# Performance work log

Measured on AMD Instinct MI355X. Metric: run time of the kernel, lower is better.

## Reference

```python
import jax, jax.numpy as jnp
import numpy as np

SCALE = 1.0  # module scale=1; dropout_p=0 so dropout is identity; selector is Identity


def setup_inputs() -> dict:
    key = jax.random.key(0)
    k0, k1, k2, k3, k4 = jax.random.split(key, 5)
    B, S, DIN, DOUT, P, R = 4, 2048, 4096, 4096, 5, 8
    x = jax.random.normal(k0, (B, S, DIN), dtype=jnp.float32)
    W = jax.random.normal(k1, (DOUT, DIN), dtype=jnp.float32) * 0.02   # nn.Linear weight [out, in]
    lora_down = jax.random.normal(k2, (P, DIN, R), dtype=jnp.float32) * 0.02
    lora_up = jax.random.normal(k3, (P, R, DOUT), dtype=jnp.float32) * 0.02
    lora_route = jax.random.normal(k4, (P, DIN, P), dtype=jnp.float32) * 0.02
    return {"x": x, "W": W, "lora_down": lora_down, "lora_up": lora_up,
            "lora_route": lora_route, "task_id": 4}


def reference(x, W, lora_down, lora_up, lora_route, task_id):
    tid = task_id  # Python int (static), tid > 1 branch
    # Routing: logits over the first (tid-1) experts using route table of task tid
    logits = jnp.einsum('bsi,ij->bsj', x, lora_route[tid - 1, :, :tid - 1])  # [B,S,tid-1]
    omegas = jax.nn.softmax(logits, axis=-1)
    # Previous experts: (lora_down[j] @ lora_up[j]).detach() -> stop_gradient.
    # Keep low-rank structure: z = x @ down  [B,S,J,R], then weight and project up.
    down_prev = jax.lax.stop_gradient(lora_down[:tid - 1])  # [J, DIN, R]
    up_prev = jax.lax.stop_gradient(lora_up[:tid - 1])      # [J, R, DOUT]
    z = jnp.einsum('bsi,jir->bsjr', x, down_prev)           # [B,S,J,R] small (R=8)
    delta_prev = jnp.einsum('bsjr,jro->bso', z * omegas[..., None], up_prev)
    # Current expert (j == tid-1): live params, no gating weight
    cur = (x @ lora_down[tid - 1]) @ lora_up[tid - 1]       # [B,S,DOUT]
    delta = SCALE * (delta_prev + cur)
    return x @ W.T + delta
```

## Files before the change

### kernel.cpp

```cpp
#include <hip/hip_runtime.h>
#include <hip/hip_bf16.h>

typedef unsigned short u16;
typedef __attribute__((ext_vector_type(8))) __bf16 bf16x8;
typedef __attribute__((ext_vector_type(4))) float f32x4;

#define DIN 4096
#define DOUT 4096
#define MROWS 8192

__device__ __forceinline__ u16 f2bf(float f) {
  unsigned int u = __float_as_uint(f);
  u += 0x7fffu + ((u >> 16) & 1u);
  return (u16)(u >> 16);
}

__device__ __forceinline__ void gl2lds16(const void* g, void* l) {
  __builtin_amdgcn_global_load_lds(
      (const __attribute__((address_space(1))) unsigned int*)g,
      (__attribute__((address_space(3))) unsigned int*)l, 16, 0, 0);
}

__global__ __launch_bounds__(256) void convw(const float* __restrict__ W,
                                             u16* __restrict__ Wb) {
  size_t i = ((size_t)blockIdx.x * 256 + threadIdx.x) * 4;
  float4 v = *(const float4*)(W + i);
  ushort4 o;
  o.x = f2bf(v.x); o.y = f2bf(v.y); o.z = f2bf(v.z); o.w = f2bf(v.w);
  *(ushort4*)(Wb + i) = o;
}

__global__ __launch_bounds__(256) void convu(const float* __restrict__ up,
                                             u16* __restrict__ Ub) {
  int n = blockIdx.x * 256 + threadIdx.x;
  union { u16 us[32]; uint4 q[4]; } o;
  #pragma unroll
  for (int c = 0; c < 32; ++c) o.us[c] = f2bf(up[(size_t)c * DOUT + n]);
  uint4* dst = (uint4*)(Ub + (size_t)n * 32);
  #pragma unroll
  for (int q = 0; q < 4; ++q) dst[q] = o.q[q];
}

__global__ __launch_bounds__(256) void wtprep(const float* __restrict__ route,
                                              const float* __restrict__ down,
                                              u16* __restrict__ Wt) {
  const int c = blockIdx.y;
  const int k0 = blockIdx.x * 1024 + threadIdx.x * 4;
  const float* route3 = route + 3 * DIN * 5;
  float v[4];
  #pragma unroll
  for (int j = 0; j < 4; ++j) {
    int k = k0 + j;
    float f;
    if (c < 3)       f = route3[(size_t)k * 5 + c];
    else if (c < 35) f = down[(size_t)((c - 3) >> 3) * DIN * 8 + (size_t)k * 8 + ((c - 3) & 7)];
    else             f = 0.f;
    v[j] = f;
  }
  ushort4 o;
  o.x = f2bf(v[0]); o.y = f2bf(v[1]); o.z = f2bf(v[2]); o.w = f2bf(v[3]);
  *(ushort4*)(Wt + (size_t)c * DIN + k0) = o;
}

__global__ __launch_bounds__(256) void coeffgemm(
    const float* __restrict__ x, const u16* __restrict__ Wt,
    u16* __restrict__ Xb, float* __restrict__ Pw) {
  __shared__ __align__(16) u16 As[128 * 64];
  __shared__ __align__(16) u16 Bs[48 * 64];
  const int tid = threadIdx.x;
  const int m0 = blockIdx.x * 128;
  const int kb = blockIdx.y * 512;
  const int lane = tid & 63;
  const int w = tid >> 6;
  const int wr = w * 32;
  const int fm = lane & 15;
  const int xr = fm & 7;
  const int qd = lane >> 4;
  const int xrow = tid >> 4;
  const int xcol = (tid & 15) * 4;
  const int aswz = (((tid & 15) >> 1) ^ (xrow & 7)) * 8 + (tid & 1) * 4;

  f32x4 acc[2][3];
  #pragma unroll
  for (int i = 0; i < 2; ++i)
    #pragma unroll
    for (int j = 0; j < 3; ++j) acc[i][j] = (f32x4){0.f, 0.f, 0.f, 0.f};

  const int bsw = ((tid & 7) ^ ((tid >> 3) & 7)) * 8;

  for (int kc = 0; kc < 512; kc += 64) {
    gl2lds16(Wt + (size_t)(tid >> 3) * DIN + kb + kc + bsw, Bs + tid * 8);
    if (tid < 128) {
      int u = 256 + tid;
      int usw = ((u & 7) ^ ((u >> 3) & 7)) * 8;
      gl2lds16(Wt + (size_t)(u >> 3) * DIN + kb + kc + usw, Bs + u * 8);
    }
    #pragma unroll
    for (int g = 0; g < 8; ++g) {
      const int row = g * 16 + xrow;
      const size_t goff = (size_t)(m0 + row) * DIN + kb + kc + xcol;
      const float4 v = *(const float4*)(x + goff);
      ushort4 b;
      b.x = f2bf(v.x); b.y = f2bf(v.y); b.z = f2bf(v.z); b.w = f2bf(v.w);
      *(ushort4*)(Xb + goff) = b;
      *(ushort4*)(As + row * 64 + aswz) = b;
    }
    __syncthreads();
    #pragma unroll
    for (int kk = 0; kk < 64; kk += 32) {
      const int q = (kk >> 3) + qd;
      bf16x8 af[2], bfr[3];
      #pragma unroll
      for (int i = 0; i < 2; ++i)
        af[i] = *(const bf16x8*)(As + (wr + i * 16 + fm) * 64 + ((q ^ xr) << 3));
      #pragma unroll
      for (int j = 0; j < 3; ++j)
        bfr[j] = *(const bf16x8*)(Bs + (j * 16 + fm) * 64 + ((q ^ xr) << 3));
      #pragma unroll
      for (int i = 0; i < 2; ++i)
        #pragma unroll
        for (int j = 0; j < 3; ++j)
          acc[i][j] = __builtin_amdgcn_mfma_f32_16x16x32_bf16(af[i], bfr[j], acc[i][j], 0, 0, 0);
    }
    __syncthreads();
  }
  const int em = (lane >> 4) * 4;
  const int en = lane & 15;
  const size_t pbase = (size_t)blockIdx.y * MROWS;
  #pragma unroll
  for (int i = 0; i < 2; ++i)
    #pragma unroll
    for (int j = 0; j < 3; ++j)
      #pragma unroll
      for (int r = 0; r < 4; ++r)
        Pw[(pbase + m0 + wr + i * 16 + em + r) * 48 + j * 16 + en] = acc[i][j][r];
}

__global__ __launch_bounds__(256) void reduce_coeff(const float* __restrict__ Pw,
                                                    u16* __restrict__ Cb) {
  const int m = blockIdx.x * 256 + threadIdx.x;
  float s[48];
  #pragma unroll
  for (int c = 0; c < 48; ++c) s[c] = 0.f;
  for (int sp = 0; sp < 8; ++sp) {
    const float4* p = (const float4*)(Pw + ((size_t)sp * MROWS + m) * 48);
    #pragma unroll
    for (int q = 0; q < 12; ++q) {
      float4 v = p[q];
      s[q * 4 + 0] += v.x; s[q * 4 + 1] += v.y;
      s[q * 4 + 2] += v.z; s[q * 4 + 3] += v.w;
    }
  }
  float mx = fmaxf(s[0], fmaxf(s[1], s[2]));
  float e0 = __expf(s[0] - mx), e1 = __expf(s[1] - mx), e2 = __expf(s[2] - mx);
  float inv = 1.f / (e0 + e1 + e2);
  float om0 = e0 * inv, om1 = e1 * inv, om2 = e2 * inv;
  union { u16 us[32]; uint4 q[4]; } o;
  #pragma unroll
  for (int c = 0; c < 32; ++c) {
    float wgt = (c < 8) ? om0 : (c < 16) ? om1 : (c < 24) ? om2 : 1.f;
    o.us[c] = f2bf(s[3 + c] * wgt);
  }
  uint4* dst = (uint4*)(Cb + (size_t)m * 32);
  #pragma unroll
  for (int q = 0; q < 4; ++q) dst[q] = o.q[q];
}

__global__ __launch_bounds__(256) void gemm_fused(
    const u16* __restrict__ Xb, const u16* __restrict__ Wb,
    const u16* __restrict__ Cb, const u16* __restrict__ Ub,
    float* __restrict__ out) {
  __shared__ __align__(16) u16 As[128 * 64];
  __shared__ __align__(16) u16 Bs[128 * 64];
  const int tid = threadIdx.x;
  const int n0 = blockIdx.x * 128;
  const int m0 = blockIdx.y * 128;
  const int lane = tid & 63;
  const int w = tid >> 6;
  const int wr = (w >> 1) * 64;
  const int wc = (w & 1) * 64;
  const int fm = lane & 15;
  const int xr = fm & 7;
  const int qd = lane >> 4;

  f32x4 acc[4][4];
  #pragma unroll
  for (int i = 0; i < 4; ++i)
    #pragma unroll
    for (int j = 0; j < 4; ++j) acc[i][j] = (f32x4){0.f, 0.f, 0.f, 0.f};

  const int srow = tid >> 3;
  const int scol = ((tid & 7) ^ (srow & 7)) * 8;
  const u16* gA = Xb + (size_t)(m0 + srow) * DIN + scol;
  const u16* gB = Wb + (size_t)(n0 + srow) * DIN + scol;
  u16* lA = As + tid * 8;
  u16* lB = Bs + tid * 8;

  for (int k0 = 0; k0 < DIN; k0 += 64) {
    #pragma unroll
    for (int it = 0; it < 4; ++it) {
      gl2lds16(gA + (size_t)it * 32 * DIN, lA + it * 2048);
      gl2lds16(gB + (size_t)it * 32 * DIN, lB + it * 2048);
    }
    gA += 64; gB += 64;
    __syncthreads();
    #pragma unroll
    for (int kk = 0; kk < 64; kk += 32) {
      const int qoff = ((kk >> 3) + qd) ^ xr;
      bf16x8 af[4], bfr[4];
      #pragma unroll
      for (int i = 0; i < 4; ++i)
        af[i] = *(const bf16x8*)(As + (wr + i * 16 + fm) * 64 + (qoff << 3));
      #pragma unroll
      for (int j = 0; j < 4; ++j)
        bfr[j] = *(const bf16x8*)(Bs + (wc + j * 16 + fm) * 64 + (qoff << 3));
      #pragma unroll
      for (int i = 0; i < 4; ++i)
        #pragma unroll
        for (int j = 0; j < 4; ++j)
          acc[i][j] = __builtin_amdgcn_mfma_f32_16x16x32_bf16(af[i], bfr[j], acc[i][j], 0, 0, 0);
    }
    __syncthreads();
  }
  {
    const int trow = tid >> 2;
    const int tcol = (tid & 3) * 8;
    #pragma unroll
    for (int it = 0; it < 2; ++it) {
      gl2lds16(Cb + (size_t)(m0 + trow + it * 64) * 32 + tcol, lA + it * 2048);
      gl2lds16(Ub + (size_t)(n0 + trow + it * 64) * 32 + tcol, lB + it * 2048);
    }
    __syncthreads();
    const int fk = qd * 8;
    bf16x8 af[4], bfr[4];
    #pragma unroll
    for (int i = 0; i < 4; ++i)
      af[i] = *(const bf16x8*)(As + (wr + i * 16 + fm) * 32 + fk);
    #pragma unroll
    for (int j = 0; j < 4; ++j)
      bfr[j] = *(const bf16x8*)(Bs + (wc + j * 16 + fm) * 32 + fk);
    #pragma unroll
    for (int i = 0; i < 4; ++i)
      #pragma unroll
      for (int j = 0; j < 4; ++j)
        acc[i][j] = __builtin_amdgcn_mfma_f32_16x16x32_bf16(af[i], bfr[j], acc[i][j], 0, 0, 0);
  }
  const int em = (lane >> 4) * 4;
  const int en = lane & 15;
  #pragma unroll
  for (int i = 0; i < 4; ++i)
    #pragma unroll
    for (int j = 0; j < 4; ++j)
      #pragma unroll
      for (int r = 0; r < 4; ++r)
        out[(size_t)(m0 + wr + i * 16 + em + r) * DOUT + (n0 + wc + j * 16 + en)] = acc[i][j][r];
}

extern "C" void kernel_launch(void* const* d_in, const int* in_sizes, int n_in,
                              void* d_out, int out_size, void* d_ws, size_t ws_size,
                              hipStream_t stream) {
  const float* x     = (const float*)d_in[0];
  const float* W     = (const float*)d_in[1];
  const float* down  = (const float*)d_in[2];
  const float* up    = (const float*)d_in[3];
  const float* route = (const float*)d_in[4];
  float* out = (float*)d_out;

  char* ws = (char*)d_ws;
  u16*   Xb = (u16*)ws;
  u16*   Wb = (u16*)(ws + 67108864);
  u16*   Cb = (u16*)(ws + 100663296);
  u16*   Ub = (u16*)(ws + 101187584);
  u16*   Wt = (u16*)(ws + 101449728);
  float* Pw = (float*)(ws + 101842944);

  convw<<<16384, 256, 0, stream>>>(W, Wb);
  convu<<<16, 256, 0, stream>>>(up, Ub);
  wtprep<<<dim3(4, 48), 256, 0, stream>>>(route, down, Wt);
  coeffgemm<<<dim3(64, 8), 256, 0, stream>>>(x, Wt, Xb, Pw);
  reduce_coeff<<<32, 256, 0, stream>>>(Pw, Cb);
  gemm_fused<<<dim3(32, 64), 256, 0, stream>>>(Xb, Wb, Cb, Ub, out);
}
```

Baseline: 569.2 us.

## Rewrite main GEMM as 256x256 tile pipelined kernel with separate x conversion

Replaces the 128x128 single-buffered GEMM with a 512-thread, 256x256-tile kernel. It uses a four-stage LDS ring of global_load_lds prefetches, explicit vmcnt waits, split barriers and setprio around the MFMA bursts, plus an XCD-aware block remap. The LoRA up-projection is folded into the last pipeline stage. x-to-bf16 conversion moves into its own kernel so coeffgemm can load bf16 directly into LDS. The aim is to hide memory latency and raise MFMA utilisation, in exchange for an extra launch and one more full pass over x.

```diff
diff --git a/kernel.cpp b/kernel.cpp
--- a/kernel.cpp
+++ b/kernel.cpp
@@ -19,6 +19,15 @@
   __builtin_amdgcn_global_load_lds(
       (const __attribute__((address_space(1))) unsigned int*)g,
       (__attribute__((address_space(3))) unsigned int*)l, 16, 0, 0);
+}
+
+__global__ __launch_bounds__(256) void convx(const float* __restrict__ x,
+                                             u16* __restrict__ Xb) {
+  size_t i = ((size_t)blockIdx.x * 256 + threadIdx.x) * 4;
+  float4 v = *(const float4*)(x + i);
+  ushort4 o;
+  o.x = f2bf(v.x); o.y = f2bf(v.y); o.z = f2bf(v.z); o.w = f2bf(v.w);
+  *(ushort4*)(Xb + i) = o;
 }
 
 __global__ __launch_bounds__(256) void convw(const float* __restrict__ W,
@@ -63,8 +72,8 @@
 }
 
 __global__ __launch_bounds__(256) void coeffgemm(
-    const float* __restrict__ x, const u16* __restrict__ Wt,
-    u16* __restrict__ Xb, float* __restrict__ Pw) {
+    const u16* __restrict__ Xb, const u16* __restrict__ Wt,
+    float* __restrict__ Pw) {
   __shared__ __align__(16) u16 As[128 * 64];
   __shared__ __align__(16) u16 Bs[48 * 64];
   const int tid = threadIdx.x;
@@ -76,9 +85,6 @@
   const int fm = lane & 15;
   const int xr = fm & 7;
   const int qd = lane >> 4;
-  const int xrow = tid >> 4;
-  const int xcol = (tid & 15) * 4;
-  const int aswz = (((tid & 15) >> 1) ^ (xrow & 7)) * 8 + (tid & 1) * 4;
 
   f32x4 acc[2][3];
   #pragma unroll
@@ -86,25 +92,21 @@
     #pragma unroll
     for (int j = 0; j < 3; ++j) acc[i][j] = (f32x4){0.f, 0.f, 0.f, 0.f};
 
-  const int bsw = ((tid & 7) ^ ((tid >> 3) & 7)) * 8;
+  const int srow = tid >> 3;
+  const int scol = ((tid & 7) ^ (srow & 7)) * 8;
+  const u16* gA = Xb + (size_t)(m0 + srow) * DIN + kb + scol;
+  u16* lA = As + tid * 8;
 
   for (int kc = 0; kc < 512; kc += 64) {
-    gl2lds16(Wt + (size_t)(tid >> 3) * DIN + kb + kc + bsw, Bs + tid * 8);
+    gl2lds16(Wt + (size_t)srow * DIN + kb + kc + scol, Bs + tid * 8);
     if (tid < 128) {
       int u = 256 + tid;
       int usw = ((u & 7) ^ ((u >> 3) & 7)) * 8;
       gl2lds16(Wt + (size_t)(u >> 3) * DIN + kb + kc + usw, Bs + u * 8);
     }
     #pragma unroll
-    for (int g = 0; g < 8; ++g) {
-      const int row = g * 16 + xrow;
-      const size_t goff = (size_t)(m0 + row) * DIN + kb + kc + xcol;
-      const float4 v = *(const float4*)(x + goff);
-      ushort4 b;
-      b.x = f2bf(v.x); b.y = f2bf(v.y); b.z = f2bf(v.z); b.w = f2bf(v.w);
-      *(ushort4*)(Xb + goff) = b;
-      *(ushort4*)(As + row * 64 + aswz) = b;
-    }
+    for (int it = 0; it < 4; ++it)
+      gl2lds16(gA + kc + (size_t)(it * 32) * DIN, lA + it * 2048);
     __syncthreads();
     #pragma unroll
     for (int kk = 0; kk < 64; kk += 32) {
@@ -166,94 +168,143 @@
   for (int q = 0; q < 4; ++q) dst[q] = o.q[q];
 }
 
-__global__ __launch_bounds__(256) void gemm_fused(
+
+#define MF(a, b, c) __builtin_amdgcn_mfma_f32_16x16x32_bf16(a, b, c, 0, 0, 0)
+
+#define MROW(A, I) \
+  acc[I][0] = MF(A, bfr0, acc[I][0]); \
+  acc[I][1] = MF(A, bfr1, acc[I][1]); \
+  acc[I][2] = MF(A, bfr2, acc[I][2]); \
+  acc[I][3] = MF(A, bfr3, acc[I][3]);
+
+#define VM4 asm volatile("s_waitcnt vmcnt(4)" ::: "memory")
+#define VM0 asm volatile("s_waitcnt vmcnt(0)" ::: "memory")
+
+#define STA(REG, KOFF) { const u16* s_ = gA + (KOFF); \
+  gl2lds16(s_, dA + (REG) * 8192); \
+  gl2lds16(s_ + 128 * 4096, dA + (REG) * 8192 + 4096); }
+#define STB(REG, KOFF) { const u16* s_ = gB + (KOFF); \
+  gl2lds16(s_, dB + (REG) * 8192); \
+  gl2lds16(s_ + 128 * 4096, dB + (REG) * 8192 + 4096); }
+#define STC { const u16* s_ = Cb + (size_t)(m0 + gr1) * 32 + kc1; \
+  gl2lds16(s_, dA); gl2lds16(s_ + 128 * 32, dA + 4096); }
+#define STU { const u16* s_ = Ub + (size_t)(n0 + gr1) * 32 + kc1; \
+  gl2lds16(s_, dB); gl2lds16(s_ + 128 * 32, dB + 4096); }
+
+#define PH(REG, IH, LOADB, ISSUE, VMX) { \
+  const u16* ap_ = sm + (REG) * 8192 + wmoff + (IH) * 2048 + off0; \
+  bf16x8 af0 = *(const bf16x8*)(ap_); \
+  bf16x8 af1 = *(const bf16x8*)(ap_ + 512); \
+  bf16x8 af2 = *(const bf16x8*)(ap_ + 1024); \
+  bf16x8 af3 = *(const bf16x8*)(ap_ + 1536); \
+  if (LOADB) { \
+    const u16* bp_ = sm + 32768 + (REG) * 8192 + wnoff + off0; \
+    bfr0 = *(const bf16x8*)(bp_); \
+    bfr1 = *(const bf16x8*)(bp_ + 512); \
+    bfr2 = *(const bf16x8*)(bp_ + 1024); \
+    bfr3 = *(const bf16x8*)(bp_ + 1536); \
+  } \
+  ISSUE; \
+  asm volatile("" ::: "memory"); \
+  __builtin_amdgcn_s_barrier(); \
+  __builtin_amdgcn_s_setprio(1); \
+  MROW(af0, (IH) * 4 + 0) \
+  MROW(af1, (IH) * 4 + 1) \
+  MROW(af2, (IH) * 4 + 2) \
+  MROW(af3, (IH) * 4 + 3) \
+  __builtin_amdgcn_s_setprio(0); \
+  VMX; \
+  asm volatile("" ::: "memory"); \
+  __builtin_amdgcn_s_barrier(); \
+}
+
+#define TILE(B, I1, I2, I3, I4, VMX) { \
+  bf16x8 bfr0, bfr1, bfr2, bfr3; \
+  PH((B) * 2 + 0, 0, 1, I1, (void)0) \
+  PH((B) * 2 + 0, 1, 0, I2, (void)0) \
+  PH((B) * 2 + 1, 0, 1, I3, (void)0) \
+  PH((B) * 2 + 1, 1, 0, I4, VMX) \
+}
+
+__global__ __launch_bounds__(512, 2) void gemm_fused8(
     const u16* __restrict__ Xb, const u16* __restrict__ Wb,
     const u16* __restrict__ Cb, const u16* __restrict__ Ub,
     float* __restrict__ out) {
-  __shared__ __align__(16) u16 As[128 * 64];
-  __shared__ __align__(16) u16 Bs[128 * 64];
+  __shared__ __align__(16) u16 sm[65536];
   const int tid = threadIdx.x;
-  const int n0 = blockIdx.x * 128;
-  const int m0 = blockIdx.y * 128;
+  const int bid = blockIdx.x;
+  const int wg = (bid & 7) * 64 + (bid >> 3);
+  const int mt = wg >> 4;
+  const int nt = wg & 15;
+  const int m0 = mt * 256;
+  const int n0 = nt * 256;
   const int lane = tid & 63;
   const int w = tid >> 6;
-  const int wr = (w >> 1) * 64;
-  const int wc = (w & 1) * 64;
+  const int wm = w >> 2;
+  const int wn = w & 3;
   const int fm = lane & 15;
-  const int xr = fm & 7;
   const int qd = lane >> 4;
-
-  f32x4 acc[4][4];
-  #pragma unroll
-  for (int i = 0; i < 4; ++i)
+  const int off0 = (fm >> 1) * 64 + (((((fm & 1) << 2) | qd)) ^ (fm >> 1)) * 8;
+  const int wmoff = wm * 4096;
+  const int wnoff = wn * 2048;
+
+  const int c1 = (tid & 7) ^ ((tid >> 3) & 7);
+  const int gr1 = 2 * (tid >> 3) + (c1 >> 2);
+  const int kc1 = (c1 & 3) * 8;
+  const u16* gA = Xb + (size_t)(m0 + gr1) * 4096 + kc1;
+  const u16* gB = Wb + (size_t)(n0 + gr1) * 4096 + kc1;
+  u16* dA = sm + tid * 8;
+  u16* dB = sm + 32768 + tid * 8;
+
+  f32x4 acc[8][4];
+  #pragma unroll
+  for (int i = 0; i < 8; ++i)
     #pragma unroll
     for (int j = 0; j < 4; ++j) acc[i][j] = (f32x4){0.f, 0.f, 0.f, 0.f};
 
-  const int srow = tid >> 3;
-  const int scol = ((tid & 7) ^ (srow & 7)) * 8;
-  const u16* gA = Xb + (size_t)(m0 + srow) * DIN + scol;
-  const u16* gB = Wb + (size_t)(n0 + srow) * DIN + scol;
-  u16* lA = As + tid * 8;
-  u16* lB = Bs + tid * 8;
-
-  for (int k0 = 0; k0 < DIN; k0 += 64) {
-    #pragma unroll
-    for (int it = 0; it < 4; ++it) {
-      gl2lds16(gA + (size_t)it * 32 * DIN, lA + it * 2048);
-      gl2lds16(gB + (size_t)it * 32 * DIN, lB + it * 2048);
+  STA(0, 0)  STB(0, 0)
+  STA(1, 32) STB(1, 32)
+  STA(2, 64) STB(2, 64)
+  VM4;
+  asm volatile("" ::: "memory");
+  __builtin_amdgcn_s_barrier();
+
+  for (int T = 0; T < 62; T += 2) {
+    TILE(0, STA(3, T * 64 + 96),  STB(3, T * 64 + 96),
+            STA(0, T * 64 + 128), STB(0, T * 64 + 128), VM4)
+    TILE(1, STA(1, T * 64 + 160), STB(1, T * 64 + 160),
+            STA(2, T * 64 + 192), STB(2, T * 64 + 192), VM4)
+  }
+  TILE(0, STA(3, 4064), STB(3, 4064), (void)0, (void)0, VM0)
+  TILE(1, STC, STU, (void)0, (void)0, VM0)
+
+  {
+    const u16* ap = sm + wmoff + off0;
+    const u16* bp = sm + 32768 + wnoff + off0;
+    bf16x8 bfr0 = *(const bf16x8*)(bp);
+    bf16x8 bfr1 = *(const bf16x8*)(bp + 512);
+    bf16x8 bfr2 = *(const bf16x8*)(bp + 1024);
+    bf16x8 bfr3 = *(const bf16x8*)(bp + 1536);
+    #pragma unroll
+    for (int i = 0; i < 8; ++i) {
+      bf16x8 a = *(const bf16x8*)(ap + i * 512);
+      acc[i][0] = MF(a, bfr0, acc[i][0]);
+      acc[i][1] = MF(a, bfr1, acc[i][1]);
+      acc[i][2] = MF(a, bfr2, acc[i][2]);
+      acc[i][3] = MF(a, bfr3, acc[i][3]);
     }
-    gA += 64; gB += 64;
-    __syncthreads();
-    #pragma unroll
-    for (int kk = 0; kk < 64; kk += 32) {
-      const int qoff = ((kk >> 3) + qd) ^ xr;
-      bf16x8 af[4], bfr[4];
-      #pragma unroll
-      for (int i = 0; i < 4; ++i)
-        af[i] = *(const bf16x8*)(As + (wr + i * 16 + fm) * 64 + (qoff << 3));
-      #pragma unroll
-      for (int j = 0; j < 4; ++j)
-        bfr[j] = *(const bf16x8*)(Bs + (wc + j * 16 + fm) * 64 + (qoff << 3));
-      #pragma unroll
-      for (int i = 0; i < 4; ++i)
-        #pragma unroll
-        for (int j = 0; j < 4; ++j)
-          acc[i][j] = __builtin_amdgcn_mfma_f32_16x16x32_bf16(af[i], bfr[j], acc[i][j], 0, 0, 0);
-    }
-    __syncthreads();
-  }
-  {
-    const int trow = tid >> 2;
-    const int tcol = (tid & 3) * 8;
-    #pragma unroll
-    for (int it = 0; it < 2; ++it) {
-      gl2lds16(Cb + (size_t)(m0 + trow + it * 64) * 32 + tcol, lA + it * 2048);
-      gl2lds16(Ub + (size_t)(n0 + trow + it * 64) * 32 + tcol, lB + it * 2048);
-    }
-    __syncthreads();
-    const int fk = qd * 8;
-    bf16x8 af[4], bfr[4];
-    #pragma unroll
-    for (int i = 0; i < 4; ++i)
-      af[i] = *(const bf16x8*)(As + (wr + i * 16 + fm) * 32 + fk);
+  }
+
+  const int em = qd * 4;
+  const int en = fm;
+  const size_t obase = (size_t)(m0 + wm * 128) * DOUT + n0 + wn * 64 + en;
+  #pragma unroll
+  for (int i = 0; i < 8; ++i)
     #pragma unroll
     for (int j = 0; j < 4; ++j)
-      bfr[j] = *(const bf16x8*)(Bs + (wc + j * 16 + fm) * 32 + fk);
-    #pragma unroll
-    for (int i = 0; i < 4; ++i)
-      #pragma unroll
-      for (int j = 0; j < 4; ++j)
-        acc[i][j] = __builtin_amdgcn_mfma_f32_16x16x32_bf16(af[i], bfr[j], acc[i][j], 0, 0, 0);
-  }
-  const int em = (lane >> 4) * 4;
-  const int en = lane & 15;
-  #pragma unroll
-  for (int i = 0; i < 4; ++i)
-    #pragma unroll
-    for (int j = 0; j < 4; ++j)
       #pragma unroll
       for (int r = 0; r < 4; ++r)
-        out[(size_t)(m0 + wr + i * 16 + em + r) * DOUT + (n0 + wc + j * 16 + en)] = acc[i][j][r];
+        out[obase + (size_t)(i * 16 + em + r) * DOUT + j * 16] = acc[i][j][r];
 }
 
 extern "C" void kernel_launch(void* const* d_in, const int* in_sizes, int n_in,
@@ -274,10 +325,11 @@
   u16*   Wt = (u16*)(ws + 101449728);
   float* Pw = (float*)(ws + 101842944);
 
+  convx<<<32768, 256, 0, stream>>>(x, Xb);
   convw<<<16384, 256, 0, stream>>>(W, Wb);
   convu<<<16, 256, 0, stream>>>(up, Ub);
   wtprep<<<dim3(4, 48), 256, 0, stream>>>(route, down, Wt);
-  coeffgemm<<<dim3(64, 8), 256, 0, stream>>>(x, Wt, Xb, Pw);
+  coeffgemm<<<dim3(64, 8), 256, 0, stream>>>(Xb, Wt, Pw);
   reduce_coeff<<<32, 256, 0, stream>>>(Pw, Cb);
-  gemm_fused<<<dim3(32, 64), 256, 0, stream>>>(Xb, Wb, Cb, Ub, out);
-}
+  gemm_fused8<<<512, 512, 0, stream>>>(Xb, Wb, Cb, Ub, out);
+}
```

Result: faster. 521.7 us (-8.3%).
